# Kernel tuning notes

Measured on AMD Instinct MI355X. Metric: run time of the kernel, lower is better.

The kernel has to match this reference:

```python
import jax, jax.numpy as jnp
import numpy as np

H, Q, D, V = 256, 64, 512, 34
L, N, T = 1024, 64, 256


def _mlp(x, W0, b0, W1, b1):
    # two-layer MLP with ELU on hidden (matches MLP with nn.ELU activation)
    return jax.nn.elu(x @ W0.T + b0) @ W1.T + b1


def _lstm_cell(x, h, c, Wih, Whh, bih, bhh):
    gates = x @ Wih.T + bih + h @ Whh.T + bhh
    i, f, g, o = jnp.split(gates, 4, axis=-1)  # PyTorch LSTMCell gate order
    i, f, o = jax.nn.sigmoid(i), jax.nn.sigmoid(f), jax.nn.sigmoid(o)
    c_new = f * c + i * jnp.tanh(g)
    h_new = o * jnp.tanh(c_new)
    return h_new, c_new


def _attn(q, key, value, mask):
    # q: [N,Q], key: [N,L,Q], value: [N,L,H], mask: [N,L]
    scores = jnp.einsum('nlq,nq->nl', key, q)
    a = jax.nn.softmax(scores, axis=-1) * mask
    a = a / jnp.sum(a, axis=-1, keepdims=True)
    return jnp.einsum('nl,nlh->nh', a, value)


def setup_inputs() -> dict:
    key = jax.random.key(0)
    ks = iter(jax.random.split(key, 64))

    def rn(shape, s=0.05):
        return jax.random.normal(next(ks), shape, jnp.float32) * s

    inp = {
        'seqs': rn((L, N, D), 1.0),
        'seq_lens': jax.random.randint(next(ks), (N,), L // 2, L + 1),
        'labels': jax.random.randint(next(ks), (T, N), 0, V),
        'emb': rn((V, H)),
        'inith': rn((3, H)),
        'initc': rn((3, H)),
    }
    in_sizes = [2 * H, H, H]
    for i in range(3):
        inp[f'Wih{i}'] = rn((4 * H, in_sizes[i]))
        inp[f'Whh{i}'] = rn((4 * H, H))
        inp[f'bih{i}'] = rn((4 * H,))
        inp[f'bhh{i}'] = rn((4 * H,))
    inp['qW0'] = rn((H, H)); inp['qb0'] = rn((H,))
    inp['qW1'] = rn((Q, H)); inp['qb1'] = rn((Q,))
    inp['kW0'] = rn((D, D)); inp['kb0'] = rn((D,))
    inp['kW1'] = rn((Q, D)); inp['kb1'] = rn((Q,))
    inp['vW0'] = rn((H, D)); inp['vb0'] = rn((H,))
    inp['vW1'] = rn((H, H)); inp['vb1'] = rn((H,))
    inp['outW'] = rn((V, 2 * H)); inp['outb'] = rn((V,))
    return inp


def reference(seqs, seq_lens, labels, emb, inith, initc,
              Wih0, Whh0, bih0, bhh0, Wih1, Whh1, bih1, bhh1,
              Wih2, Whh2, bih2, bhh2,
              qW0, qb0, qW1, qb1, kW0, kb0, kW1, kb1,
              vW0, vb0, vW1, vb1, outW, outb):
    T_, N_ = labels.shape
    L_ = seqs.shape[0]
    lstm = [(Wih0, Whh0, bih0, bhh0), (Wih1, Whh1, bih1, bhh1), (Wih2, Whh2, bih2, bhh2)]

    char_input = emb[labels]                                   # [T,N,H]
    key = _mlp(seqs, kW0, kb0, kW1, kb1).transpose(1, 0, 2)    # [N,L,Q]
    value = _mlp(seqs, vW0, vb0, vW1, vb1).transpose(1, 0, 2)  # [N,L,H]
    mask = (jnp.arange(L_)[None, :] < seq_lens[:, None]).astype(seqs.dtype)

    h = jnp.tile(inith[:, None, :], (1, N_, 1))  # [3,N,H]
    c = jnp.tile(initc[:, None, :], (1, N_, 1))
    q = _mlp(h[2], qW0, qb0, qW1, qb1)
    prev_ctx = _attn(q, key, value, mask)

    def step(carry, x_t):
        h, c, ctx = carry
        xin = jnp.concatenate([ctx, x_t], axis=1)  # [N,2H]
        hs, cs = [], []
        for i in range(3):
            nh, nc = _lstm_cell(xin, h[i], c[i], *lstm[i])
            hs.append(nh); cs.append(nc)
            xin = nh
        h = jnp.stack(hs); c = jnp.stack(cs)
        q = _mlp(h[2], qW0, qb0, qW1, qb1)
        ctx = _attn(q, key, value, mask)
        out = jnp.concatenate([ctx, h[2]], axis=1) @ outW.T + outb  # [N,V]
        return (h, c, ctx), out

    _, outs = jax.lax.scan(step, (h, c, prev_ctx), char_input)
    return outs  # [T,N,V]
```

## Files before the change

### kernel.cpp

```cpp
#include <hip/hip_runtime.h>
#include <cstddef>

#define DEV static __device__ __forceinline__
typedef unsigned long long ull;

DEV float b2f(unsigned short u){ unsigned int i=((unsigned int)u)<<16; float f; __builtin_memcpy(&f,&i,4); return f; }
DEV float lo16(unsigned int u){ unsigned int i=u<<16; float f; __builtin_memcpy(&f,&i,4); return f; }
DEV float hi16(unsigned int u){ unsigned int i=u&0xffff0000u; float f; __builtin_memcpy(&f,&i,4); return f; }
DEV unsigned short f2b(float f){ unsigned int i; __builtin_memcpy(&i,&f,4); unsigned int r=(i+0x7fffu+((i>>16)&1u))>>16; return (unsigned short)r; }
DEV float sigf(float x){ return 1.f/(1.f+__expf(-x)); }
DEV float eluf(float x){ return x>0.f ? x : (__expf(x)-1.f); }
DEV float gload(const void* p, long i, int f32){
  return f32 ? ((const float*)p)[i] : b2f(((const unsigned short*)p)[i]);
}
DEV ull pk(float f, unsigned tag){ unsigned b; __builtin_memcpy(&b,&f,4); return ((ull)tag<<32)|b; }
DEV float upk(ull u){ unsigned b=(unsigned)u; float f; __builtin_memcpy(&f,&b,4); return f; }
DEV void ast64(ull* p, ull v){ __hip_atomic_store(p, v, __ATOMIC_RELAXED, __HIP_MEMORY_SCOPE_AGENT); }
DEV ull ald64(const ull* p){ return __hip_atomic_load(p, __ATOMIC_RELAXED, __HIP_MEMORY_SCOPE_AGENT); }

__global__ __launch_bounds__(64) void sniff(const void* __restrict__ seqs,
                                            const void* __restrict__ seq_lens,
                                            int* __restrict__ flags)
{
  __shared__ int cnt;
  if (threadIdx.x==0) cnt=0;
  __syncthreads();
  const unsigned short* u = (const unsigned short*)seqs;
  int sane=0;
  for (int i=threadIdx.x;i<1024;i+=64){
    int e = (u[i]>>7)&0xFF;
    if (e>=0x70 && e<=0x8F) sane++;
  }
  atomicAdd(&cnt, sane);
  __syncthreads();
  if (threadIdx.x==0){
    flags[0] = (cnt < 820) ? 1 : 0;
    const int* s = (const int*)seq_lens;
    flags[1] = ((s[1]|s[3]|s[5]|s[7])==0) ? 1 : 0;
  }
}

__global__ __launch_bounds__(256) void prep_transpose(
    const void* __restrict__ Wih0, const void* __restrict__ Whh0,
    const void* __restrict__ Wih1, const void* __restrict__ Whh1,
    const void* __restrict__ Wih2, const void* __restrict__ Whh2,
    const void* __restrict__ kW0,  const void* __restrict__ kW1,
    const void* __restrict__ vW0,  const void* __restrict__ vW1,
    const void* __restrict__ qW0,  const void* __restrict__ qW1,
    const void* __restrict__ bih0, const void* __restrict__ bhh0,
    const void* __restrict__ bih1, const void* __restrict__ bhh1,
    const void* __restrict__ bih2, const void* __restrict__ bhh2,
    const void* __restrict__ outW, const void* __restrict__ inith,
    const void* __restrict__ initc, const void* __restrict__ qb0,
    const void* __restrict__ qb1,  const void* __restrict__ outb,
    const int* __restrict__ flags,
    unsigned short* __restrict__ Wl0, unsigned short* __restrict__ Wl1,
    unsigned short* __restrict__ Wl2,
    unsigned short* __restrict__ kW0T, unsigned short* __restrict__ kW1T,
    unsigned short* __restrict__ vW0T, unsigned short* __restrict__ vW1T,
    unsigned short* __restrict__ qW0v, unsigned short* __restrict__ qW1v,
    float* __restrict__ bsum,
    unsigned short* __restrict__ outWc, unsigned short* __restrict__ inithc,
    unsigned short* __restrict__ initcc, unsigned short* __restrict__ qb0c,
    unsigned short* __restrict__ qb1c,  unsigned short* __restrict__ outbc)
{
  const int f32 = flags[0];
  int idx = blockIdx.x*256 + threadIdx.x;
  if (idx < 524288){ int r=idx&131071, k=r>>8, gi=r&255;
    int g = ((gi>>6)<<8) + ((idx>>17)<<6) + (gi&63);
    Wl0[idx] = f2b((k<256)? gload(Wih0,(long)g*512+k,f32) : gload(Whh0,(long)g*256+(k-256),f32)); return; }
  idx -= 524288;
  if (idx < 524288){ int r=idx&131071, k=r>>8, gi=r&255;
    int g = ((gi>>6)<<8) + ((idx>>17)<<6) + (gi&63);
    Wl1[idx] = f2b((k<256)? gload(Wih1,(long)g*256+k,f32) : gload(Whh1,(long)g*256+(k-256),f32)); return; }
  idx -= 524288;
  if (idx < 524288){ int r=idx&131071, k=r>>8, gi=r&255;
    int g = ((gi>>6)<<8) + ((idx>>17)<<6) + (gi&63);
    Wl2[idx] = f2b((k<256)? gload(Wih2,(long)g*256+k,f32) : gload(Whh2,(long)g*256+(k-256),f32)); return; }
  idx -= 524288;
  if (idx < 262144){ int k=idx>>9, j=idx&511; kW0T[idx]=f2b(gload(kW0,(long)j*512+k,f32)); return; }
  idx -= 262144;
  if (idx < 32768){ int k=idx>>6, j=idx&63; kW1T[idx]=f2b(gload(kW1,(long)j*512+k,f32)); return; }
  idx -= 32768;
  if (idx < 131072){ int k=idx>>8, j=idx&255; vW0T[idx]=f2b(gload(vW0,(long)j*512+k,f32)); return; }
  idx -= 131072;
  if (idx < 65536){ int k=idx>>8, j=idx&255; vW1T[idx]=f2b(gload(vW1,(long)j*256+k,f32)); return; }
  idx -= 65536;
  if (idx < 65536){
    int k8=idx>>11, j=(idx>>3)&255, kk=idx&7; int k=k8*8+kk;
    qW0v[idx]=f2b(gload(qW0,(long)j*256+k,f32)); return; }
  idx -= 65536;
  if (idx < 16384){
    int k8=idx>>11, qc=(idx>>5)&63, kk=idx&31; int k=k8*32+kk;
    qW1v[idx]=f2b(gload(qW1,(long)qc*256+k,f32)); return; }
  idx -= 16384;
  if (idx < 3072){ int l=idx>>10, r=idx&1023, pp=r>>8, gi=r&255;
    int g = ((gi>>6)<<8) + (pp<<6) + (gi&63);
    const void* bi = (l==0)?bih0:((l==1)?bih1:bih2);
    const void* bh = (l==0)?bhh0:((l==1)?bhh1:bhh2);
    bsum[idx] = gload(bi,g,f32)+gload(bh,g,f32); return; }
  idx -= 3072;
  if (idx < 17408){ outWc[idx]=f2b(gload(outW,idx,f32)); return; }
  idx -= 17408;
  if (idx < 768){ inithc[idx]=f2b(gload(inith,idx,f32)); return; }
  idx -= 768;
  if (idx < 768){ initcc[idx]=f2b(gload(initc,idx,f32)); return; }
  idx -= 768;
  if (idx < 256){ qb0c[idx]=f2b(gload(qb0,idx,f32)); return; }
  idx -= 256;
  if (idx < 64){ qb1c[idx]=f2b(gload(qb1,idx,f32)); return; }
  idx -= 64;
  if (idx < 34){ outbc[idx]=f2b(gload(outb,idx,f32)); return; }
}

__global__ __launch_bounds__(256) void prep_ge(
    const void* __restrict__ emb,
    const void* __restrict__ Wih0,
    const int* __restrict__ flags,
    float* __restrict__ gep)
{
  __shared__ float ev[256];
  const int f32 = flags[0];
  const int v = blockIdx.x, tid = threadIdx.x;
  ev[tid] = gload(emb,(long)v*256+tid,f32);
  __syncthreads();
  #pragma unroll
  for (int j=0;j<4;j++){
    const int g = tid*4+j;
    float a = 0.f;
    #pragma unroll 4
    for (int k=0;k<256;k++) a += ev[k]*gload(Wih0,(long)g*512+256+k,f32);
    int pp = (g>>6)&3, gi = ((g>>8)<<6)|(g&63);
    gep[((size_t)pp*34+v)*256+gi] = a;
  }
}

__global__ __launch_bounds__(256) void key_mlp(
    const void* __restrict__ seqs,
    const unsigned short* __restrict__ kW0T, const void* __restrict__ kb0,
    const unsigned short* __restrict__ kW1T, const void* __restrict__ kb1,
    const int* __restrict__ flags,
    unsigned short* __restrict__ keyT)
{
  __shared__ float Xt[16*512];
  __shared__ unsigned short Hd[16*512];
  const int f32 = flags[0];
  const int tid = threadIdx.x;
  const int R0 = blockIdx.x*16;
  for (int i=tid;i<8192;i+=256) Xt[i] = gload(seqs,(long)R0*512+i,f32);
  __syncthreads();
  {
    const int j0 = 2*tid;
    float acc0[16], acc1[16];
    #pragma unroll
    for (int r=0;r<16;r++){ acc0[r]=0.f; acc1[r]=0.f; }
    for (int k=0;k<512;k++){
      ushort2 w = *reinterpret_cast<const ushort2*>(kW0T + (size_t)k*512 + j0);
      float w0=b2f(w.x), w1=b2f(w.y);
      #pragma unroll
      for (int r=0;r<16;r++){ float x = Xt[r*512+k]; acc0[r]+=x*w0; acc1[r]+=x*w1; }
    }
    float b0v=gload(kb0,j0,f32), b1v=gload(kb0,j0+1,f32);
    #pragma unroll
    for (int r=0;r<16;r++){
      Hd[r*512+j0]   = f2b(eluf(acc0[r]+b0v));
      Hd[r*512+j0+1] = f2b(eluf(acc1[r]+b1v));
    }
  }
  __syncthreads();
  {
    const int j = tid & 63;
    const int rbase = tid >> 6;
    float acc[4] = {0.f,0.f,0.f,0.f};
    for (int k=0;k<512;k++){
      float w = b2f(kW1T[(size_t)k*64 + j]);
      #pragma unroll
      for (int m=0;m<4;m++) acc[m] += b2f(Hd[(rbase+4*m)*512 + k]) * w;
    }
    float bv = gload(kb1,j,f32);
    #pragma unroll
    for (int m=0;m<4;m++){
      int R = R0 + rbase + 4*m;
      int l = R >> 6, n = R & 63;
      keyT[((size_t)(n*64 + j))*1024 + l] = f2b(acc[m]+bv);
    }
  }
}

__global__ __launch_bounds__(256) void value_mlp(
    const void* __restrict__ seqs,
    const unsigned short* __restrict__ vW0T, const void* __restrict__ vb0,
    const unsigned short* __restrict__ vW1T, const void* __restrict__ vb1,
    const int* __restrict__ flags,
    unsigned short* __restrict__ value)
{
  __shared__ float Xt[16*512];
  __shared__ float Hd[16*256];
  const int f32 = flags[0];
  const int tid = threadIdx.x;
  const int R0 = blockIdx.x*16;
  for (int i=tid;i<8192;i+=256) Xt[i] = gload(seqs,(long)R0*512+i,f32);
  __syncthreads();
  {
    const int j0 = 2*(tid & 127);
    const int rh = tid >> 7;
    float acc0[8], acc1[8];
    #pragma unroll
    for (int r=0;r<8;r++){ acc0[r]=0.f; acc1[r]=0.f; }
    for (int k=0;k<512;k++){
      ushort2 w = *reinterpret_cast<const ushort2*>(vW0T + (size_t)k*256 + j0);
      float w0=b2f(w.x), w1=b2f(w.y);
      #pragma unroll
      for (int r=0;r<8;r++){ float x = Xt[(rh*8+r)*512+k]; acc0[r]+=x*w0; acc1[r]+=x*w1; }
    }
    float b0v=gload(vb0,j0,f32), b1v=gload(vb0,j0+1,f32);
    #pragma unroll
    for (int r=0;r<8;r++){
      Hd[(rh*8+r)*256+j0]   = eluf(acc0[r]+b0v);
      Hd[(rh*8+r)*256+j0+1] = eluf(acc1[r]+b1v);
    }
  }
  __syncthreads();
  {
    const int j = tid;
    float acc[16];
    #pragma unroll
    for (int r=0;r<16;r++) acc[r]=0.f;
    for (int k=0;k<256;k++){
      float w = b2f(vW1T[(size_t)k*256 + j]);
      #pragma unroll
      for (int r=0;r<16;r++) acc[r] += Hd[r*256+k]*w;
    }
    float bv = gload(vb1,j,f32);
    #pragma unroll
    for (int r=0;r<16;r++){
      int R = R0 + r; int l = R>>6, n = R&63;
      value[((size_t)n*1024 + l)*256 + j] = f2b(acc[r]+bv);
    }
  }
}

__global__ __launch_bounds__(256) void zero_hbuf(ull* __restrict__ f){
  int i = blockIdx.x*256 + threadIdx.x;
  if (i < 115200) f[i] = 0;
}

__global__ __launch_bounds__(512, 1) void speller(
    const unsigned short* __restrict__ keyT,
    const unsigned short* __restrict__ value,
    const unsigned short* __restrict__ Wl0,
    const unsigned short* __restrict__ Wl1,
    const unsigned short* __restrict__ Wl2,
    const unsigned short* __restrict__ qW0v,
    const unsigned short* __restrict__ qW1v,
    const float* __restrict__ bsum_p,
    const float* __restrict__ gep,
    const unsigned short* __restrict__ inithc,
    const unsigned short* __restrict__ initcc,
    const unsigned short* __restrict__ qb0c,
    const unsigned short* __restrict__ qb1c,
    const unsigned short* __restrict__ outWc,
    const unsigned short* __restrict__ outbc,
    const int* __restrict__ labels,
    const int* __restrict__ seq_lens,
    const int* __restrict__ dflags,
    ull* __restrict__ hbw,
    void* __restrict__ out)
{
  extern __shared__ char smem_dyn[];
  unsigned short* vlds = (unsigned short*)smem_dyn;

  __shared__ float sacc[4096];
  __shared__ float inc[512];
  __shared__ float garr[256];
  __shared__ float h0[256], h1[256], h2[256], ctx[256];
  __shared__ float cloc[3][64];
  __shared__ float hsl[3][64];
  __shared__ float xq[256];
  __shared__ float qv[64];
  __shared__ float earr[256];
  __shared__ float red[16];
  __shared__ float wf[4];
  __shared__ float pcl[256];
  __shared__ float statl[8];

  const int tid = threadIdx.x;
  const int n = blockIdx.x >> 2;
  const int p = blockIdx.x & 3;
  const int f32o = dflags[0];
  const int i64 = dflags[1];
  const int slen = i64 ? seq_lens[2*n] : seq_lens[n];

  ull* mb   = hbw + (size_t)n*1800;
  ull* H0w  = mb;
  ull* H1w  = mb + 256;
  ull* H2w  = mb + 512;
  ull* PCw  = mb + 768;
  ull* STw  = mb + 1792;

  {
    const uint4* src = (const uint4*)(value + ((size_t)n*1024 + p*256)*256);
    uint4* dst = (uint4*)vlds;
    for (int i=tid;i<16384;i+=512) dst[i] = src[i];
  }
  if (tid < 256){ h0[tid]=b2f(inithc[tid]); h1[tid]=b2f(inithc[256+tid]); h2[tid]=b2f(inithc[512+tid]); }
  if (tid < 64){
    cloc[0][tid]=b2f(initcc[p*64+tid]);
    cloc[1][tid]=b2f(initcc[256+p*64+tid]);
    cloc[2][tid]=b2f(initcc[512+p*64+tid]);
  }
  __syncthreads();

  auto lstm = [&](const unsigned short* W, const float* bs, const float* ger,
                  int layer, ull* Hw, unsigned tag){
    const int go8 = tid & 31, ks = tid >> 5;
    const unsigned short* wp = W + (size_t)p*131072 + (size_t)ks*32*256 + go8*8;
    const float* xin = inc + ks*32;
    float a0=0.f,a1=0.f,a2=0.f,a3=0.f,a4=0.f,a5=0.f,a6=0.f,a7=0.f;
    #pragma unroll 16
    for (int k=0;k<32;k++){
      float x = xin[k];
      uint4 w = *reinterpret_cast<const uint4*>(wp + (size_t)k*256);
      a0 += x*lo16(w.x); a1 += x*hi16(w.x);
      a2 += x*lo16(w.y); a3 += x*hi16(w.y);
      a4 += x*lo16(w.z); a5 += x*hi16(w.z);
      a6 += x*lo16(w.w); a7 += x*hi16(w.w);
    }
    float* sb = sacc + ks*256 + go8*8;
    sb[0]=a0; sb[1]=a1; sb[2]=a2; sb[3]=a3; sb[4]=a4; sb[5]=a5; sb[6]=a6; sb[7]=a7;
    __syncthreads();
    if (tid < 256){
      float s = bs[tid] + (ger ? ger[tid] : 0.f);
      #pragma unroll
      for (int u=0;u<16;u++) s += sacc[u*256+tid];
      garr[tid] = s;
    }
    __syncthreads();
    if (tid < 64){
      float gi=garr[tid], gf=garr[64+tid], gg=garr[128+tid], go=garr[192+tid];
      float cc = sigf(gf)*cloc[layer][tid] + sigf(gi)*tanhf(gg);
      float hh = sigf(go)*tanhf(cc);
      cloc[layer][tid]=cc;
      hsl[layer][tid]=hh;
      ast64(Hw + p*64 + tid, pk(hh, tag));
    }
  };

  auto gather_h = [&](const ull* Hw, int layer, unsigned tag, float* hdst,
                      const float* nexth){
    __syncthreads();
    if (tid < 256){
      int sp = tid >> 6; float v;
      if (sp == p) v = hsl[layer][tid & 63];
      else { const ull* w = Hw + tid; ull u = ald64(w);
             while ((unsigned)(u>>32) != tag) u = ald64(w);
             v = upk(u); }
      hdst[tid] = v;
      if (nexth){ inc[tid] = v; inc[256+tid] = nexth[tid]; }
    }
    __syncthreads();
  };

  auto attn = [&](unsigned tag){
    {
      const int j = tid & 255, kh = tid >> 8;
      const uint4* qp = (const uint4*)qW0v + (size_t)(kh*16)*256 + j;
      float a = 0.f;
      #pragma unroll
      for (int k8=0;k8<16;k8++){
        uint4 w = qp[(size_t)k8*256];
        const float* hb = h2 + kh*128 + k8*8;
        a += hb[0]*lo16(w.x)+hb[1]*hi16(w.x)
           + hb[2]*lo16(w.y)+hb[3]*hi16(w.y)
           + hb[4]*lo16(w.z)+hb[5]*hi16(w.z)
           + hb[6]*lo16(w.w)+hb[7]*hi16(w.w);
      }
      sacc[kh*256 + j] = a;
    }
    __syncthreads();
    if (tid < 256) xq[tid] = eluf(sacc[tid]+sacc[256+tid] + b2f(qb0c[tid]));
    __syncthreads();
    {
      const int qc = tid & 63, k8 = tid >> 6;
      const uint4* qp = (const uint4*)qW1v + (size_t)(k8*64+qc)*4;
      float a = 0.f;
      #pragma unroll
      for (int u=0;u<4;u++){
        uint4 w = qp[u];
        const float* xb = xq + k8*32 + u*8;
        a += xb[0]*lo16(w.x)+xb[1]*hi16(w.x)
           + xb[2]*lo16(w.y)+xb[3]*hi16(w.y)
           + xb[4]*lo16(w.z)+xb[5]*hi16(w.z)
           + xb[6]*lo16(w.w)+xb[7]*hi16(w.w);
      }
      sacc[k8*64+qc] = a;
    }
    __syncthreads();
    if (tid < 64){
      float s=0.f;
      #pragma unroll
      for (int u=0;u<8;u++) s += sacc[u*64+tid];
      qv[tid] = s + b2f(qb1c[tid]);
    }
    __syncthreads();
    {
      const int lp = tid & 127, qh = tid >> 7;
      float a0=0.f,a1=0.f;
      const unsigned short* kp = keyT + (size_t)n*65536 + (size_t)qh*16*1024 + p*256 + 2*lp;
      #pragma unroll 8
      for (int q=0;q<16;q++){
        ushort2 w = *reinterpret_cast<const ushort2*>(kp + (size_t)q*1024);
        float qq = qv[qh*16+q];
        a0 += qq*b2f(w.x); a1 += qq*b2f(w.y);
      }
      sacc[qh*256+2*lp]=a0; sacc[qh*256+2*lp+1]=a1;
    }
    __syncthreads();
    float pmax, psum;
    {
      float s = -1e30f;
      if (tid < 256){
        s = sacc[tid]+sacc[256+tid]+sacc[512+tid]+sacc[768+tid];
        if (p*256+tid >= slen) s = -1e30f;
      }
      float m = s;
      #pragma unroll
      for (int off=32; off; off>>=1) m = fmaxf(m, __shfl_xor(m, off));
      if ((tid&63)==0) red[tid>>6] = m;
      __syncthreads();
      pmax = fmaxf(fmaxf(red[0],red[1]),fmaxf(red[2],red[3]));
      float e = 0.f;
      if (tid < 256){
        e = (p*256+tid < slen) ? __expf(s - pmax) : 0.f;
        earr[tid] = e;
      }
      float ss = e;
      #pragma unroll
      for (int off=32; off; off>>=1) ss += __shfl_xor(ss, off);
      if ((tid&63)==0) red[8+(tid>>6)] = ss;
      __syncthreads();
      psum = red[8]+red[9]+red[10]+red[11];
    }
    {
      const int hp = tid & 127, lq = tid >> 7;
      float a0=0.f,a1=0.f;
      const unsigned short* vp = vlds + (size_t)(lq*64)*256 + 2*hp;
      #pragma unroll 8
      for (int l=0;l<64;l++){
        ushort2 w = *reinterpret_cast<const ushort2*>(vp + (size_t)l*256);
        float e = earr[lq*64+l];
        a0 += e*b2f(w.x); a1 += e*b2f(w.y);
      }
      sacc[lq*256+2*hp]=a0; sacc[lq*256+2*hp+1]=a1;
    }
    __syncthreads();
    if (tid < 256){
      float v = sacc[tid]+sacc[256+tid]+sacc[512+tid]+sacc[768+tid];
      pcl[tid] = v;
      ast64(PCw + p*256 + tid, pk(v, tag));
    }
    if (tid == 0){ ast64(STw + p*2, pk(pmax, tag)); ast64(STw + p*2 + 1, pk(psum, tag)); }
    if (tid < 8){
      int q = tid >> 1, ix = tid & 1; float v;
      if (q == p) v = ix ? psum : pmax;
      else { const ull* w = STw + q*2 + ix; ull u = ald64(w);
             while ((unsigned)(u>>32) != tag) u = ald64(w);
             v = upk(u); }
      statl[tid] = v;
    }
    __syncthreads();
    if (tid == 0){
      float m0=statl[0], s0=statl[1], m1=statl[2], s1=statl[3];
      float m2=statl[4], s2=statl[5], m3=statl[6], s3=statl[7];
      float M = fmaxf(fmaxf(m0,m1),fmaxf(m2,m3));
      float w0=__expf(m0-M), w1=__expf(m1-M), w2=__expf(m2-M), w3=__expf(m3-M);
      float inv = 1.f/(s0*w0+s1*w1+s2*w2+s3*w3);
      wf[0]=w0*inv; wf[1]=w1*inv; wf[2]=w2*inv; wf[3]=w3*inv;
    }
    __syncthreads();
    if (tid < 256){
      const int q0=(p+1)&3, q1=(p+2)&3, q2=(p+3)&3;
      const ull* w0 = PCw + q0*256 + tid;
      const ull* w1 = PCw + q1*256 + tid;
      const ull* w2 = PCw + q2*256 + tid;
      ull u0=ald64(w0), u1=ald64(w1), u2=ald64(w2);
      while ((unsigned)(u0>>32) != tag) u0 = ald64(w0);
      while ((unsigned)(u1>>32) != tag) u1 = ald64(w1);
      while ((unsigned)(u2>>32) != tag) u2 = ald64(w2);
      float acc = pcl[tid]*wf[p] + upk(u0)*wf[q0] + upk(u1)*wf[q1] + upk(u2)*wf[q2];
      ctx[tid] = acc;
      inc[tid] = acc;
      inc[256+tid] = h0[tid];
    }
    __syncthreads();
  };

  attn(1);

  for (int t=0;t<256;t++){
    const unsigned tb = 4*(unsigned)t;
    const int lab = i64 ? labels[2*(t*64+n)] : labels[t*64+n];
    lstm(Wl0, bsum_p + p*256, gep + ((size_t)p*34+lab)*256, 0, H0w, tb+2);
    gather_h(H0w, 0, tb+2, h0, h1);
    lstm(Wl1, bsum_p + 1024 + p*256, nullptr, 1, H1w, tb+3);
    gather_h(H1w, 1, tb+3, h1, h2);
    lstm(Wl2, bsum_p + 2048 + p*256, nullptr, 2, H2w, tb+4);
    gather_h(H2w, 2, tb+4, h2, nullptr);
    attn(tb+5);
    {
      const int ri = tid >> 6, kk = tid & 63;
      const int r = 4*ri + p;
      float acc = 0.f;
      const unsigned short* wr = outWc + (size_t)r*512 + kk;
      #pragma unroll
      for (int s=0;s<4;s++) acc += ctx[s*64+kk]*b2f(wr[s*64]);
      #pragma unroll
      for (int s=0;s<4;s++) acc += h2[s*64+kk]*b2f(wr[256+s*64]);
      #pragma unroll
      for (int off=32; off>0; off>>=1) acc += __shfl_down(acc, off);
      if (kk==0){
        float v = acc + b2f(outbc[r]);
        size_t oi = ((size_t)(t*64+n))*34 + r;
        if (f32o) ((float*)out)[oi]=v; else ((unsigned short*)out)[oi]=f2b(v);
      }
      if (p < 2 && tid < 64){
        const int r2 = 32+p;
        float a2=0.f;
        const unsigned short* wr2 = outWc + (size_t)r2*512 + tid;
        #pragma unroll
        for (int s=0;s<4;s++) a2 += ctx[s*64+tid]*b2f(wr2[s*64]);
        #pragma unroll
        for (int s=0;s<4;s++) a2 += h2[s*64+tid]*b2f(wr2[256+s*64]);
        #pragma unroll
        for (int off=32; off>0; off>>=1) a2 += __shfl_down(a2, off);
        if (tid==0){
          float v = a2 + b2f(outbc[r2]);
          size_t oi = ((size_t)(t*64+n))*34 + r2;
          if (f32o) ((float*)out)[oi]=v; else ((unsigned short*)out)[oi]=f2b(v);
        }
      }
    }
  }
}

extern "C" void kernel_launch(void* const* d_in, const int* in_sizes, int n_in,
                              void* d_out, int out_size, void* d_ws, size_t ws_size,
                              hipStream_t stream) {
  const void* seqs  = d_in[0];
  const int* seq_lens = (const int*)d_in[1];
  const int* labels   = (const int*)d_in[2];
  const void* emb   = d_in[3];
  const void* inith = d_in[4];
  const void* initc = d_in[5];
  const void* Wih0 = d_in[6];  const void* Whh0 = d_in[7];
  const void* bih0 = d_in[8];  const void* bhh0 = d_in[9];
  const void* Wih1 = d_in[10]; const void* Whh1 = d_in[11];
  const void* bih1 = d_in[12]; const void* bhh1 = d_in[13];
  const void* Wih2 = d_in[14]; const void* Whh2 = d_in[15];
  const void* bih2 = d_in[16]; const void* bhh2 = d_in[17];
  const void* qW0 = d_in[18];  const void* qb0 = d_in[19];
  const void* qW1 = d_in[20];  const void* qb1 = d_in[21];
  const void* kW0 = d_in[22];  const void* kb0 = d_in[23];
  const void* kW1 = d_in[24];  const void* kb1 = d_in[25];
  const void* vW0 = d_in[26];  const void* vb0 = d_in[27];
  const void* vW1 = d_in[28];  const void* vb1 = d_in[29];
  const void* outW = d_in[30]; const void* outb = d_in[31];

  char* ws = (char*)d_ws;
  unsigned short* keyT  = (unsigned short*)(ws);
  unsigned short* value = (unsigned short*)(ws + 8388608);
  unsigned short* Wl0   = (unsigned short*)(ws + 41943040);
  unsigned short* Wl1   = (unsigned short*)(ws + 42991616);
  unsigned short* Wl2   = (unsigned short*)(ws + 44040192);
  unsigned short* kW0T  = (unsigned short*)(ws + 45088768);
  unsigned short* kW1T  = (unsigned short*)(ws + 45613056);
  unsigned short* vW0T  = (unsigned short*)(ws + 45678592);
  unsigned short* vW1T  = (unsigned short*)(ws + 45940736);
  unsigned short* qW0v  = (unsigned short*)(ws + 46071808);
  unsigned short* qW1v  = (unsigned short*)(ws + 46202880);
  float*          bsum  = (float*)(ws + 46235648);
  float*          gep   = (float*)(ws + 46247936);
  unsigned short* outWc = (unsigned short*)(ws + 46387200);
  unsigned short* inithc= (unsigned short*)(ws + 46422016);
  unsigned short* initcc= (unsigned short*)(ws + 46423552);
  unsigned short* qb0c  = (unsigned short*)(ws + 46425088);
  unsigned short* qb1c  = (unsigned short*)(ws + 46425600);
  unsigned short* outbc = (unsigned short*)(ws + 46425728);
  int*            dflags= (int*)(ws + 46425856);
  ull* hbw = (ull*)(ws + 45088768);

  sniff<<<dim3(1), dim3(64), 0, stream>>>(seqs, seq_lens, dflags);
  prep_transpose<<<dim3(8472), dim3(256), 0, stream>>>(
      Wih0,Whh0,Wih1,Whh1,Wih2,Whh2, kW0,kW1,vW0,vW1,qW0,qW1,
      bih0,bhh0,bih1,bhh1,bih2,bhh2,
      outW,inith,initc,qb0,qb1,outb, dflags,
      Wl0,Wl1,Wl2,kW0T,kW1T,vW0T,vW1T,qW0v,qW1v,bsum,
      outWc,inithc,initcc,qb0c,qb1c,outbc);
  prep_ge<<<dim3(34), dim3(256), 0, stream>>>(emb, Wih0, dflags, gep);
  key_mlp<<<dim3(4096), dim3(256), 0, stream>>>(seqs, kW0T, kb0, kW1T, kb1, dflags, keyT);
  value_mlp<<<dim3(4096), dim3(256), 0, stream>>>(seqs, vW0T, vb0, vW1T, vb1, dflags, value);
  zero_hbuf<<<dim3(450), dim3(256), 0, stream>>>(hbw);
  hipFuncSetAttribute((const void*)speller, hipFuncAttributeMaxDynamicSharedMemorySize, 131072);
  speller<<<dim3(256), dim3(512), 131072, stream>>>(
      keyT, value, Wl0, Wl1, Wl2, qW0v, qW1v, bsum, gep,
      inithc, initcc, qb0c, qb1c, outWc, outbc, labels, seq_lens, dflags,
      hbw, d_out);
}
```

Baseline: 8.160 ms.

## Double speller block to 1024 threads and re-split per-step matvecs

Raises the recurrent speller kernel from 512 to 1024 threads per block. The LSTM gate matvec, the query MLP, the key-score and the value-context reductions are re-partitioned so each thread handles half as many elements, and the partial-sum reductions grow accordingly. The qW1 weight layout in prep is changed to match the new split. The aim is to cut per-step latency on the serial time loop by using more lanes, at the cost of extra shared-memory reduction work and heavier barriers across 16 waves. It also risks register pressure under the tighter launch bound.

```diff
diff --git a/kernel.cpp b/kernel.cpp
--- a/kernel.cpp
+++ b/kernel.cpp
@@ -91,7 +91,7 @@
     qW0v[idx]=f2b(gload(qW0,(long)j*256+k,f32)); return; }
   idx -= 65536;
   if (idx < 16384){
-    int k8=idx>>11, qc=(idx>>5)&63, kk=idx&31; int k=k8*32+kk;
+    int s=idx>>10, qc=(idx>>4)&63, kk=idx&15; int k=s*16+kk;
     qW1v[idx]=f2b(gload(qW1,(long)qc*256+k,f32)); return; }
   idx -= 16384;
   if (idx < 3072){ int l=idx>>10, r=idx&1023, pp=r>>8, gi=r&255;
@@ -245,7 +245,7 @@
   if (i < 115200) f[i] = 0;
 }
 
-__global__ __launch_bounds__(512, 1) void speller(
+__global__ __launch_bounds__(1024, 4) void speller(
     const unsigned short* __restrict__ keyT,
     const unsigned short* __restrict__ value,
     const unsigned short* __restrict__ Wl0,
@@ -301,7 +301,7 @@
   {
     const uint4* src = (const uint4*)(value + ((size_t)n*1024 + p*256)*256);
     uint4* dst = (uint4*)vlds;
-    for (int i=tid;i<16384;i+=512) dst[i] = src[i];
+    for (int i=tid;i<16384;i+=1024) dst[i] = src[i];
   }
   if (tid < 256){ h0[tid]=b2f(inithc[tid]); h1[tid]=b2f(inithc[256+tid]); h2[tid]=b2f(inithc[512+tid]); }
   if (tid < 64){
@@ -313,21 +313,19 @@
 
   auto lstm = [&](const unsigned short* W, const float* bs, const float* ger,
                   int layer, ull* Hw, unsigned tag){
-    const int go8 = tid & 31, ks = tid >> 5;
-    const unsigned short* wp = W + (size_t)p*131072 + (size_t)ks*32*256 + go8*8;
+    const int g4 = tid & 63, ks = tid >> 6;
+    const unsigned short* wp = W + (size_t)p*131072 + (size_t)ks*32*256 + g4*4;
     const float* xin = inc + ks*32;
-    float a0=0.f,a1=0.f,a2=0.f,a3=0.f,a4=0.f,a5=0.f,a6=0.f,a7=0.f;
+    float a0=0.f,a1=0.f,a2=0.f,a3=0.f;
     #pragma unroll 16
     for (int k=0;k<32;k++){
       float x = xin[k];
-      uint4 w = *reinterpret_cast<const uint4*>(wp + (size_t)k*256);
+      uint2 w = *reinterpret_cast<const uint2*>(wp + (size_t)k*256);
       a0 += x*lo16(w.x); a1 += x*hi16(w.x);
       a2 += x*lo16(w.y); a3 += x*hi16(w.y);
-      a4 += x*lo16(w.z); a5 += x*hi16(w.z);
-      a6 += x*lo16(w.w); a7 += x*hi16(w.w);
-    }
-    float* sb = sacc + ks*256 + go8*8;
-    sb[0]=a0; sb[1]=a1; sb[2]=a2; sb[3]=a3; sb[4]=a4; sb[5]=a5; sb[6]=a6; sb[7]=a7;
+    }
+    float* sb = sacc + ks*256 + g4*4;
+    sb[0]=a0; sb[1]=a1; sb[2]=a2; sb[3]=a3;
     __syncthreads();
     if (tid < 256){
       float s = bs[tid] + (ger ? ger[tid] : 0.f);
@@ -364,12 +362,12 @@
   auto attn = [&](unsigned tag){
     {
       const int j = tid & 255, kh = tid >> 8;
-      const uint4* qp = (const uint4*)qW0v + (size_t)(kh*16)*256 + j;
+      const uint4* qp = (const uint4*)qW0v + (size_t)(kh*8)*256 + j;
       float a = 0.f;
       #pragma unroll
-      for (int k8=0;k8<16;k8++){
+      for (int k8=0;k8<8;k8++){
         uint4 w = qp[(size_t)k8*256];
-        const float* hb = h2 + kh*128 + k8*8;
+        const float* hb = h2 + kh*64 + k8*8;
         a += hb[0]*lo16(w.x)+hb[1]*hi16(w.x)
            + hb[2]*lo16(w.y)+hb[3]*hi16(w.y)
            + hb[4]*lo16(w.z)+hb[5]*hi16(w.z)
@@ -378,39 +376,39 @@
       sacc[kh*256 + j] = a;
     }
     __syncthreads();
-    if (tid < 256) xq[tid] = eluf(sacc[tid]+sacc[256+tid] + b2f(qb0c[tid]));
+    if (tid < 256) xq[tid] = eluf(sacc[tid]+sacc[256+tid]+sacc[512+tid]+sacc[768+tid] + b2f(qb0c[tid]));
     __syncthreads();
     {
-      const int qc = tid & 63, k8 = tid >> 6;
-      const uint4* qp = (const uint4*)qW1v + (size_t)(k8*64+qc)*4;
+      const int qc = tid & 63, s = tid >> 6;
+      const uint4* qp = (const uint4*)qW1v + (size_t)(s*64+qc)*2;
       float a = 0.f;
       #pragma unroll
-      for (int u=0;u<4;u++){
+      for (int u=0;u<2;u++){
         uint4 w = qp[u];
-        const float* xb = xq + k8*32 + u*8;
+        const float* xb = xq + s*16 + u*8;
         a += xb[0]*lo16(w.x)+xb[1]*hi16(w.x)
            + xb[2]*lo16(w.y)+xb[3]*hi16(w.y)
            + xb[4]*lo16(w.z)+xb[5]*hi16(w.z)
            + xb[6]*lo16(w.w)+xb[7]*hi16(w.w);
       }
-      sacc[k8*64+qc] = a;
+      sacc[s*64+qc] = a;
     }
     __syncthreads();
     if (tid < 64){
       float s=0.f;
       #pragma unroll
-      for (int u=0;u<8;u++) s += sacc[u*64+tid];
+      for (int u=0;u<16;u++) s += sacc[u*64+tid];
       qv[tid] = s + b2f(qb1c[tid]);
     }
     __syncthreads();
     {
       const int lp = tid & 127, qh = tid >> 7;
       float a0=0.f,a1=0.f;
-      const unsigned short* kp = keyT + (size_t)n*65536 + (size_t)qh*16*1024 + p*256 + 2*lp;
-      #pragma unroll 8
-      for (int q=0;q<16;q++){
+      const unsigned short* kp = keyT + (size_t)n*65536 + (size_t)qh*8*1024 + p*256 + 2*lp;
+      #pragma unroll
+      for (int q=0;q<8;q++){
         ushort2 w = *reinterpret_cast<const ushort2*>(kp + (size_t)q*1024);
-        float qq = qv[qh*16+q];
+        float qq = qv[qh*8+q];
         a0 += qq*b2f(w.x); a1 += qq*b2f(w.y);
       }
       sacc[qh*256+2*lp]=a0; sacc[qh*256+2*lp+1]=a1;
@@ -420,13 +418,14 @@
     {
       float s = -1e30f;
       if (tid < 256){
-        s = sacc[tid]+sacc[256+tid]+sacc[512+tid]+sacc[768+tid];
+        s = sacc[tid]+sacc[256+tid]+sacc[512+tid]+sacc[768+tid]
+          + sacc[1024+tid]+sacc[1280+tid]+sacc[1536+tid]+sacc[1792+tid];
         if (p*256+tid >= slen) s = -1e30f;
       }
       float m = s;
       #pragma unroll
       for (int off=32; off; off>>=1) m = fmaxf(m, __shfl_xor(m, off));
-      if ((tid&63)==0) red[tid>>6] = m;
+      if (tid < 256 && (tid&63)==0) red[tid>>6] = m;
       __syncthreads();
       pmax = fmaxf(fmaxf(red[0],red[1]),fmaxf(red[2],red[3]));
       float e = 0.f;
@@ -437,25 +436,26 @@
       float ss = e;
       #pragma unroll
       for (int off=32; off; off>>=1) ss += __shfl_xor(ss, off);
-      if ((tid&63)==0) red[8+(tid>>6)] = ss;
+      if (tid < 256 && (tid&63)==0) red[8+(tid>>6)] = ss;
       __syncthreads();
       psum = red[8]+red[9]+red[10]+red[11];
     }
     {
       const int hp = tid & 127, lq = tid >> 7;
       float a0=0.f,a1=0.f;
-      const unsigned short* vp = vlds + (size_t)(lq*64)*256 + 2*hp;
+      const unsigned short* vp = vlds + (size_t)(lq*32)*256 + 2*hp;
       #pragma unroll 8
-      for (int l=0;l<64;l++){
+      for (int l=0;l<32;l++){
         ushort2 w = *reinterpret_cast<const ushort2*>(vp + (size_t)l*256);
-        float e = earr[lq*64+l];
+        float e = earr[lq*32+l];
         a0 += e*b2f(w.x); a1 += e*b2f(w.y);
       }
       sacc[lq*256+2*hp]=a0; sacc[lq*256+2*hp+1]=a1;
     }
     __syncthreads();
     if (tid < 256){
-      float v = sacc[tid]+sacc[256+tid]+sacc[512+tid]+sacc[768+tid];
+      float v = sacc[tid]+sacc[256+tid]+sacc[512+tid]+sacc[768+tid]
+              + sacc[1024+tid]+sacc[1280+tid]+sacc[1536+tid]+sacc[1792+tid];
       pcl[tid] = v;
       ast64(PCw + p*256 + tid, pk(v, tag));
     }
@@ -507,7 +507,7 @@
     lstm(Wl2, bsum_p + 2048 + p*256, nullptr, 2, H2w, tb+4);
     gather_h(H2w, 2, tb+4, h2, nullptr);
     attn(tb+5);
-    {
+    if (tid < 512){
       const int ri = tid >> 6, kk = tid & 63;
       const int r = 4*ri + p;
       float acc = 0.f;
@@ -601,7 +601,7 @@
   value_mlp<<<dim3(4096), dim3(256), 0, stream>>>(seqs, vW0T, vb0, vW1T, vb1, dflags, value);
   zero_hbuf<<<dim3(450), dim3(256), 0, stream>>>(hbw);
   hipFuncSetAttribute((const void*)speller, hipFuncAttributeMaxDynamicSharedMemorySize, 131072);
-  speller<<<dim3(256), dim3(512), 131072, stream>>>(
+  speller<<<dim3(256), dim3(1024), 131072, stream>>>(
       keyT, value, Wl0, Wl1, Wl2, qW0v, qW1v, bsum, gep,
       inithc, initcc, qb0c, qb1c, outWc, outbc, labels, seq_lens, dflags,
       hbw, d_out);
```

Result: slower. 13.99 ms (+71.5%).

## Fuse cross-block h polling into LSTM matvec with shuffle broadcast

Applied to the files above, without the earlier changes.

Layers 1 and 2 of the LSTM now poll the previous layer's published h directly inside the matvec. Each wave broadcasts the polled values to its lanes with shuffles instead of first gathering them into shared memory behind an extra barrier. This removes one __syncthreads and one LDS round trip per layer per step. The gate activations are raised in wave priority so their results are published to other blocks sooner, and the qW1 layout is reshuffled for the query MLP second layer. The risk is that waves for different k-slices each spin-wait separately, and the lane mapping and layout changes must still match.

```diff
diff --git a/kernel.cpp b/kernel.cpp
--- a/kernel.cpp
+++ b/kernel.cpp
@@ -91,7 +91,7 @@
     qW0v[idx]=f2b(gload(qW0,(long)j*256+k,f32)); return; }
   idx -= 65536;
   if (idx < 16384){
-    int k8=idx>>11, qc=(idx>>5)&63, kk=idx&31; int k=k8*32+kk;
+    int s=idx>>10, qc=(idx>>4)&63, kk=idx&15; int k=s*16+kk;
     qW1v[idx]=f2b(gload(qW1,(long)qc*256+k,f32)); return; }
   idx -= 16384;
   if (idx < 3072){ int l=idx>>10, r=idx&1023, pp=r>>8, gi=r&255;
@@ -275,7 +275,6 @@
   __shared__ float garr[256];
   __shared__ float h0[256], h1[256], h2[256], ctx[256];
   __shared__ float cloc[3][64];
-  __shared__ float hsl[3][64];
   __shared__ float xq[256];
   __shared__ float qv[64];
   __shared__ float earr[256];
@@ -311,8 +310,8 @@
   }
   __syncthreads();
 
-  auto lstm = [&](const unsigned short* W, const float* bs, const float* ger,
-                  int layer, ull* Hw, unsigned tag){
+  auto lstm_lds = [&](const unsigned short* W, const float* bs, const float* ger,
+                      int layer, ull* Hw, unsigned tag){
     const int go8 = tid & 31, ks = tid >> 5;
     const unsigned short* wp = W + (size_t)p*131072 + (size_t)ks*32*256 + go8*8;
     const float* xin = inc + ks*32;
@@ -337,26 +336,68 @@
     }
     __syncthreads();
     if (tid < 64){
+      __builtin_amdgcn_s_setprio(1);
       float gi=garr[tid], gf=garr[64+tid], gg=garr[128+tid], go=garr[192+tid];
       float cc = sigf(gf)*cloc[layer][tid] + sigf(gi)*tanhf(gg);
       float hh = sigf(go)*tanhf(cc);
       cloc[layer][tid]=cc;
-      hsl[layer][tid]=hh;
       ast64(Hw + p*64 + tid, pk(hh, tag));
+      __builtin_amdgcn_s_setprio(0);
     }
   };
 
-  auto gather_h = [&](const ull* Hw, int layer, unsigned tag, float* hdst,
-                      const float* nexth){
+  auto lstm_poll = [&](const unsigned short* W, const float* bs,
+                       const ull* Xw, unsigned xtag, const float* hprev,
+                       float* xdst, int layer, ull* Hw, unsigned tag){
+    const int go8 = tid & 31, ks = tid >> 5;
+    const int lane = tid & 63, wv = tid >> 6;
+    float xv;
+    if (wv < 4){
+      const ull* wd = Xw + tid;
+      ull u = ald64(wd);
+      while ((unsigned)(u>>32) != xtag) u = ald64(wd);
+      xv = upk(u);
+    } else {
+      xv = hprev[tid - 256];
+    }
+    const unsigned short* wp = W + (size_t)p*131072 + (size_t)ks*32*256 + go8*8;
+    float a0=0.f,a1=0.f,a2=0.f,a3=0.f,a4=0.f,a5=0.f,a6=0.f,a7=0.f;
+    #pragma unroll 16
+    for (int k=0;k<32;k++){
+      float x = __shfl(xv, (lane & 32) | k);
+      uint4 w = *reinterpret_cast<const uint4*>(wp + (size_t)k*256);
+      a0 += x*lo16(w.x); a1 += x*hi16(w.x);
+      a2 += x*lo16(w.y); a3 += x*hi16(w.y);
+      a4 += x*lo16(w.z); a5 += x*hi16(w.z);
+      a6 += x*lo16(w.w); a7 += x*hi16(w.w);
+    }
+    float* sb = sacc + ks*256 + go8*8;
+    sb[0]=a0; sb[1]=a1; sb[2]=a2; sb[3]=a3; sb[4]=a4; sb[5]=a5; sb[6]=a6; sb[7]=a7;
+    if (wv < 4) xdst[tid] = xv;
     __syncthreads();
     if (tid < 256){
-      int sp = tid >> 6; float v;
-      if (sp == p) v = hsl[layer][tid & 63];
-      else { const ull* w = Hw + tid; ull u = ald64(w);
-             while ((unsigned)(u>>32) != tag) u = ald64(w);
-             v = upk(u); }
-      hdst[tid] = v;
-      if (nexth){ inc[tid] = v; inc[256+tid] = nexth[tid]; }
+      float s = bs[tid];
+      #pragma unroll
+      for (int u=0;u<16;u++) s += sacc[u*256+tid];
+      garr[tid] = s;
+    }
+    __syncthreads();
+    if (tid < 64){
+      __builtin_amdgcn_s_setprio(1);
+      float gi=garr[tid], gf=garr[64+tid], gg=garr[128+tid], go=garr[192+tid];
+      float cc = sigf(gf)*cloc[layer][tid] + sigf(gi)*tanhf(gg);
+      float hh = sigf(go)*tanhf(cc);
+      cloc[layer][tid]=cc;
+      ast64(Hw + p*64 + tid, pk(hh, tag));
+      __builtin_amdgcn_s_setprio(0);
+    }
+  };
+
+  auto gather_h2 = [&](unsigned tag){
+    if (tid < 256){
+      const ull* w = H2w + tid; ull u = ald64(w);
+      while ((unsigned)(u>>32) != tag) u = ald64(w);
+      h2[tid] = upk(u);
     }
     __syncthreads();
   };
@@ -381,19 +422,23 @@
     if (tid < 256) xq[tid] = eluf(sacc[tid]+sacc[256+tid] + b2f(qb0c[tid]));
     __syncthreads();
     {
-      const int qc = tid & 63, k8 = tid >> 6;
-      const uint4* qp = (const uint4*)qW1v + (size_t)(k8*64+qc)*4;
+      const int qc = tid & 63, s = tid >> 6;
+      const uint4* qp = (const uint4*)qW1v + (size_t)(2*s*64+qc)*2;
       float a = 0.f;
       #pragma unroll
-      for (int u=0;u<4;u++){
-        uint4 w = qp[u];
-        const float* xb = xq + k8*32 + u*8;
-        a += xb[0]*lo16(w.x)+xb[1]*hi16(w.x)
-           + xb[2]*lo16(w.y)+xb[3]*hi16(w.y)
-           + xb[4]*lo16(w.z)+xb[5]*hi16(w.z)
-           + xb[6]*lo16(w.w)+xb[7]*hi16(w.w);
-      }
-      sacc[k8*64+qc] = a;
+      for (int half=0;half<2;half++){
+        const uint4* qph = qp + (size_t)half*64*2;
+        #pragma unroll
+        for (int u=0;u<2;u++){
+          uint4 w = qph[u];
+          const float* xb = xq + s*32 + half*16 + u*8;
+          a += xb[0]*lo16(w.x)+xb[1]*hi16(w.x)
+             + xb[2]*lo16(w.y)+xb[3]*hi16(w.y)
+             + xb[4]*lo16(w.z)+xb[5]*hi16(w.z)
+             + xb[6]*lo16(w.w)+xb[7]*hi16(w.w);
+        }
+      }
+      sacc[s*64+qc] = a;
     }
     __syncthreads();
     if (tid < 64){
@@ -500,12 +545,10 @@
   for (int t=0;t<256;t++){
     const unsigned tb = 4*(unsigned)t;
     const int lab = i64 ? labels[2*(t*64+n)] : labels[t*64+n];
-    lstm(Wl0, bsum_p + p*256, gep + ((size_t)p*34+lab)*256, 0, H0w, tb+2);
-    gather_h(H0w, 0, tb+2, h0, h1);
-    lstm(Wl1, bsum_p + 1024 + p*256, nullptr, 1, H1w, tb+3);
-    gather_h(H1w, 1, tb+3, h1, h2);
-    lstm(Wl2, bsum_p + 2048 + p*256, nullptr, 2, H2w, tb+4);
-    gather_h(H2w, 2, tb+4, h2, nullptr);
+    lstm_lds(Wl0, bsum_p + p*256, gep + ((size_t)p*34+lab)*256, 0, H0w, tb+2);
+    lstm_poll(Wl1, bsum_p + 1024 + p*256, H0w, tb+2, h1, h0, 1, H1w, tb+3);
+    lstm_poll(Wl2, bsum_p + 2048 + p*256, H1w, tb+3, h2, h1, 2, H2w, tb+4);
+    gather_h2(tb+4);
     attn(tb+5);
     {
       const int ri = tid >> 6, kk = tid & 63;
```

Result: no change. 8.173 ms (+0.2%).

## Relayout LSTM and query weights for per-thread dot products, cache layer-1 weights in registers

Applied to the files above, without the earlier changes.

Rewrites the weight pre-pack so each thread owns one gate row half and streams contiguous 16-byte chunks. Partial sums are then combined with wave shuffles instead of LDS staging and extra barriers, and the gate nonlinearity is done in-wave. Layer-1 LSTM weights are kept resident in 32 uint4 registers per thread across all timesteps, avoiding re-reading them each step. The query MLP gets the same shuffle-reduction treatment. This trades higher register pressure, which may lower occupancy or cause spills, for fewer barriers and less shared-memory traffic.

```diff
diff --git a/kernel.cpp b/kernel.cpp
--- a/kernel.cpp
+++ b/kernel.cpp
@@ -66,16 +66,25 @@
 {
   const int f32 = flags[0];
   int idx = blockIdx.x*256 + threadIdx.x;
-  if (idx < 524288){ int r=idx&131071, k=r>>8, gi=r&255;
-    int g = ((gi>>6)<<8) + ((idx>>17)<<6) + (gi&63);
+  if (idx < 524288){ int pp=idx>>17, r=idx&131071;
+    int it8=r>>12, ln=(r>>3)&511, e=r&7;
+    int j=ln>>3, gi=(ln>>1)&3, half=ln&1;
+    int g = gi*256 + pp*64 + j;
+    int k = half*256 + it8*8 + e;
     Wl0[idx] = f2b((k<256)? gload(Wih0,(long)g*512+k,f32) : gload(Whh0,(long)g*256+(k-256),f32)); return; }
   idx -= 524288;
-  if (idx < 524288){ int r=idx&131071, k=r>>8, gi=r&255;
-    int g = ((gi>>6)<<8) + ((idx>>17)<<6) + (gi&63);
+  if (idx < 524288){ int pp=idx>>17, r=idx&131071;
+    int it8=r>>12, ln=(r>>3)&511, e=r&7;
+    int j=ln>>3, gi=(ln>>1)&3, half=ln&1;
+    int g = gi*256 + pp*64 + j;
+    int k = half*256 + it8*8 + e;
     Wl1[idx] = f2b((k<256)? gload(Wih1,(long)g*256+k,f32) : gload(Whh1,(long)g*256+(k-256),f32)); return; }
   idx -= 524288;
-  if (idx < 524288){ int r=idx&131071, k=r>>8, gi=r&255;
-    int g = ((gi>>6)<<8) + ((idx>>17)<<6) + (gi&63);
+  if (idx < 524288){ int pp=idx>>17, r=idx&131071;
+    int it8=r>>12, ln=(r>>3)&511, e=r&7;
+    int j=ln>>3, gi=(ln>>1)&3, half=ln&1;
+    int g = gi*256 + pp*64 + j;
+    int k = half*256 + it8*8 + e;
     Wl2[idx] = f2b((k<256)? gload(Wih2,(long)g*256+k,f32) : gload(Whh2,(long)g*256+(k-256),f32)); return; }
   idx -= 524288;
   if (idx < 262144){ int k=idx>>9, j=idx&511; kW0T[idx]=f2b(gload(kW0,(long)j*512+k,f32)); return; }
@@ -87,11 +96,13 @@
   if (idx < 65536){ int k=idx>>8, j=idx&255; vW1T[idx]=f2b(gload(vW1,(long)j*256+k,f32)); return; }
   idx -= 65536;
   if (idx < 65536){
-    int k8=idx>>11, j=(idx>>3)&255, kk=idx&7; int k=k8*8+kk;
+    int k8=idx>>12, ln=(idx>>3)&511, e=idx&7;
+    int j=ln>>1, half=ln&1; int k=half*128 + k8*8 + e;
     qW0v[idx]=f2b(gload(qW0,(long)j*256+k,f32)); return; }
   idx -= 65536;
   if (idx < 16384){
-    int k8=idx>>11, qc=(idx>>5)&63, kk=idx&31; int k=k8*32+kk;
+    int g=idx>>12, ln=(idx>>3)&511, e=idx&7;
+    int qc=ln>>3, s8=ln&7; int k=s8*32 + g*8 + e;
     qW1v[idx]=f2b(gload(qW1,(long)qc*256+k,f32)); return; }
   idx -= 16384;
   if (idx < 3072){ int l=idx>>10, r=idx&1023, pp=r>>8, gi=r&255;
@@ -270,12 +281,12 @@
   extern __shared__ char smem_dyn[];
   unsigned short* vlds = (unsigned short*)smem_dyn;
 
-  __shared__ float sacc[4096];
-  __shared__ float inc[512];
-  __shared__ float garr[256];
+  __shared__ float sacc[1024];
+  __shared__ __align__(16) float xb[512];
   __shared__ float h0[256], h1[256], h2[256], ctx[256];
   __shared__ float cloc[3][64];
-  __shared__ float hsl[3][64];
+  __shared__ float hown[3][64];
+  __shared__ float bsl[3][256];
   __shared__ float xq[256];
   __shared__ float qv[64];
   __shared__ float earr[256];
@@ -309,98 +320,125 @@
     cloc[1][tid]=b2f(initcc[256+p*64+tid]);
     cloc[2][tid]=b2f(initcc[512+p*64+tid]);
   }
-  __syncthreads();
-
-  auto lstm = [&](const unsigned short* W, const float* bs, const float* ger,
-                  int layer, ull* Hw, unsigned tag){
-    const int go8 = tid & 31, ks = tid >> 5;
-    const unsigned short* wp = W + (size_t)p*131072 + (size_t)ks*32*256 + go8*8;
-    const float* xin = inc + ks*32;
-    float a0=0.f,a1=0.f,a2=0.f,a3=0.f,a4=0.f,a5=0.f,a6=0.f,a7=0.f;
-    #pragma unroll 16
-    for (int k=0;k<32;k++){
-      float x = xin[k];
-      uint4 w = *reinterpret_cast<const uint4*>(wp + (size_t)k*256);
-      a0 += x*lo16(w.x); a1 += x*hi16(w.x);
-      a2 += x*lo16(w.y); a3 += x*hi16(w.y);
-      a4 += x*lo16(w.z); a5 += x*hi16(w.z);
-      a6 += x*lo16(w.w); a7 += x*hi16(w.w);
-    }
-    float* sb = sacc + ks*256 + go8*8;
-    sb[0]=a0; sb[1]=a1; sb[2]=a2; sb[3]=a3; sb[4]=a4; sb[5]=a5; sb[6]=a6; sb[7]=a7;
-    __syncthreads();
-    if (tid < 256){
-      float s = bs[tid] + (ger ? ger[tid] : 0.f);
-      #pragma unroll
-      for (int u=0;u<16;u++) s += sacc[u*256+tid];
-      garr[tid] = s;
-    }
-    __syncthreads();
-    if (tid < 64){
-      float gi=garr[tid], gf=garr[64+tid], gg=garr[128+tid], go=garr[192+tid];
-      float cc = sigf(gf)*cloc[layer][tid] + sigf(gi)*tanhf(gg);
-      float hh = sigf(go)*tanhf(cc);
-      cloc[layer][tid]=cc;
-      hsl[layer][tid]=hh;
-      ast64(Hw + p*64 + tid, pk(hh, tag));
+  for (int i=tid;i<768;i+=512){ int l=i>>8, gx=i&255; bsl[l][gx]=bsum_p[l*1024 + p*256 + gx]; }
+  uint4 w1r[32];
+  {
+    const unsigned short* wp1 = Wl1 + (size_t)p*131072 + tid*8;
+    #pragma unroll
+    for (int i=0;i<32;i++) w1r[i] = *reinterpret_cast<const uint4*>(wp1 + (size_t)i*4096);
+  }
+  __syncthreads();
+
+  const int half = tid & 1;
+  const int gidx = ((tid>>1)&3)*64 + (tid>>3);
+  const int lb   = (tid & 63) & ~7;
+
+  auto lstm_stream = [&](const unsigned short* W, int layer, const float* ger,
+                         ull* Hw, unsigned tag){
+    const float* xs = xb + half*256;
+    const unsigned short* wp = W + (size_t)p*131072 + tid*8;
+    float a = 0.f;
+    #pragma unroll 8
+    for (int it8=0; it8<32; it8++){
+      uint4 w = *reinterpret_cast<const uint4*>(wp + (size_t)it8*4096);
+      float4 x0 = *reinterpret_cast<const float4*>(xs + it8*8);
+      float4 x1 = *reinterpret_cast<const float4*>(xs + it8*8 + 4);
+      a += x0.x*lo16(w.x)+x0.y*hi16(w.x)+x0.z*lo16(w.y)+x0.w*hi16(w.y)
+         + x1.x*lo16(w.z)+x1.y*hi16(w.z)+x1.z*lo16(w.w)+x1.w*hi16(w.w);
+    }
+    a += __shfl_xor(a, 1);
+    float gsum = a + bsl[layer][gidx] + (ger ? ger[gidx] : 0.f);
+    float g_i = __shfl(gsum, lb+0);
+    float g_f = __shfl(gsum, lb+2);
+    float g_g = __shfl(gsum, lb+4);
+    float g_o = __shfl(gsum, lb+6);
+    if ((tid&7)==0){
+      __builtin_amdgcn_s_setprio(1);
+      int jj = tid>>3;
+      float cc = sigf(g_f)*cloc[layer][jj] + sigf(g_i)*tanhf(g_g);
+      float hh = sigf(g_o)*tanhf(cc);
+      cloc[layer][jj]=cc; hown[layer][jj]=hh;
+      ast64(Hw + p*64 + jj, pk(hh, tag));
+      __builtin_amdgcn_s_setprio(0);
     }
   };
 
-  auto gather_h = [&](const ull* Hw, int layer, unsigned tag, float* hdst,
-                      const float* nexth){
+  auto lstm_reg = [&](int layer, ull* Hw, unsigned tag){
+    const float* xs = xb + half*256;
+    float a = 0.f;
+    #pragma unroll
+    for (int it8=0; it8<32; it8++){
+      uint4 w = w1r[it8];
+      float4 x0 = *reinterpret_cast<const float4*>(xs + it8*8);
+      float4 x1 = *reinterpret_cast<const float4*>(xs + it8*8 + 4);
+      a += x0.x*lo16(w.x)+x0.y*hi16(w.x)+x0.z*lo16(w.y)+x0.w*hi16(w.y)
+         + x1.x*lo16(w.z)+x1.y*hi16(w.z)+x1.z*lo16(w.w)+x1.w*hi16(w.w);
+    }
+    a += __shfl_xor(a, 1);
+    float gsum = a + bsl[layer][gidx];
+    float g_i = __shfl(gsum, lb+0);
+    float g_f = __shfl(gsum, lb+2);
+    float g_g = __shfl(gsum, lb+4);
+    float g_o = __shfl(gsum, lb+6);
+    if ((tid&7)==0){
+      __builtin_amdgcn_s_setprio(1);
+      int jj = tid>>3;
+      float cc = sigf(g_f)*cloc[layer][jj] + sigf(g_i)*tanhf(g_g);
+      float hh = sigf(g_o)*tanhf(cc);
+      cloc[layer][jj]=cc; hown[layer][jj]=hh;
+      ast64(Hw + p*64 + jj, pk(hh, tag));
+      __builtin_amdgcn_s_setprio(0);
+    }
+  };
+
+  auto fill_from = [&](const ull* Hw, unsigned tag, int layer, float* harr,
+                       const float* hnext){
     __syncthreads();
     if (tid < 256){
       int sp = tid >> 6; float v;
-      if (sp == p) v = hsl[layer][tid & 63];
+      if (sp == p) v = hown[layer][tid & 63];
       else { const ull* w = Hw + tid; ull u = ald64(w);
              while ((unsigned)(u>>32) != tag) u = ald64(w);
              v = upk(u); }
-      hdst[tid] = v;
-      if (nexth){ inc[tid] = v; inc[256+tid] = nexth[tid]; }
+      harr[tid] = v;
+      if (hnext){ xb[tid] = v; xb[256+tid] = hnext[tid]; }
     }
     __syncthreads();
   };
 
   auto attn = [&](unsigned tag){
     {
-      const int j = tid & 255, kh = tid >> 8;
-      const uint4* qp = (const uint4*)qW0v + (size_t)(kh*16)*256 + j;
+      const int j = tid>>1;
       float a = 0.f;
       #pragma unroll
       for (int k8=0;k8<16;k8++){
-        uint4 w = qp[(size_t)k8*256];
-        const float* hb = h2 + kh*128 + k8*8;
+        uint4 w = ((const uint4*)qW0v)[k8*512 + tid];
+        const float* hb = h2 + half*128 + k8*8;
         a += hb[0]*lo16(w.x)+hb[1]*hi16(w.x)
            + hb[2]*lo16(w.y)+hb[3]*hi16(w.y)
            + hb[4]*lo16(w.z)+hb[5]*hi16(w.z)
            + hb[6]*lo16(w.w)+hb[7]*hi16(w.w);
       }
-      sacc[kh*256 + j] = a;
-    }
-    __syncthreads();
-    if (tid < 256) xq[tid] = eluf(sacc[tid]+sacc[256+tid] + b2f(qb0c[tid]));
+      a += __shfl_xor(a, 1);
+      if (half==0) xq[j] = eluf(a + b2f(qb0c[j]));
+    }
     __syncthreads();
     {
-      const int qc = tid & 63, k8 = tid >> 6;
-      const uint4* qp = (const uint4*)qW1v + (size_t)(k8*64+qc)*4;
+      const int qc = tid>>3, s8 = tid&7;
       float a = 0.f;
       #pragma unroll
-      for (int u=0;u<4;u++){
-        uint4 w = qp[u];
-        const float* xb = xq + k8*32 + u*8;
-        a += xb[0]*lo16(w.x)+xb[1]*hi16(w.x)
-           + xb[2]*lo16(w.y)+xb[3]*hi16(w.y)
-           + xb[4]*lo16(w.z)+xb[5]*hi16(w.z)
-           + xb[6]*lo16(w.w)+xb[7]*hi16(w.w);
-      }
-      sacc[k8*64+qc] = a;
-    }
-    __syncthreads();
-    if (tid < 64){
-      float s=0.f;
-      #pragma unroll
-      for (int u=0;u<8;u++) s += sacc[u*64+tid];
-      qv[tid] = s + b2f(qb1c[tid]);
+      for (int g=0;g<4;g++){
+        uint4 w = ((const uint4*)qW1v)[g*512 + tid];
+        const float* xs8 = xq + s8*32 + g*8;
+        a += xs8[0]*lo16(w.x)+xs8[1]*hi16(w.x)
+           + xs8[2]*lo16(w.y)+xs8[3]*hi16(w.y)
+           + xs8[4]*lo16(w.z)+xs8[5]*hi16(w.z)
+           + xs8[6]*lo16(w.w)+xs8[7]*hi16(w.w);
+      }
+      a += __shfl_xor(a, 1);
+      a += __shfl_xor(a, 2);
+      a += __shfl_xor(a, 4);
+      if (s8==0) qv[qc] = a + b2f(qb1c[qc]);
     }
     __syncthreads();
     {
@@ -489,8 +527,8 @@
       while ((unsigned)(u2>>32) != tag) u2 = ald64(w2);
       float acc = pcl[tid]*wf[p] + upk(u0)*wf[q0] + upk(u1)*wf[q1] + upk(u2)*wf[q2];
       ctx[tid] = acc;
-      inc[tid] = acc;
-      inc[256+tid] = h0[tid];
+      xb[tid] = acc;
+      xb[256+tid] = h0[tid];
     }
     __syncthreads();
   };
@@ -500,12 +538,13 @@
   for (int t=0;t<256;t++){
     const unsigned tb = 4*(unsigned)t;
     const int lab = i64 ? labels[2*(t*64+n)] : labels[t*64+n];
-    lstm(Wl0, bsum_p + p*256, gep + ((size_t)p*34+lab)*256, 0, H0w, tb+2);
-    gather_h(H0w, 0, tb+2, h0, h1);
-    lstm(Wl1, bsum_p + 1024 + p*256, nullptr, 1, H1w, tb+3);
-    gather_h(H1w, 1, tb+3, h1, h2);
-    lstm(Wl2, bsum_p + 2048 + p*256, nullptr, 2, H2w, tb+4);
-    gather_h(H2w, 2, tb+4, h2, nullptr);
+    const float* ger = gep + ((size_t)p*34+lab)*256;
+    lstm_stream(Wl0, 0, ger, H0w, tb+2);
+    fill_from(H0w, tb+2, 0, h0, h1);
+    lstm_reg(1, H1w, tb+3);
+    fill_from(H1w, tb+3, 1, h1, h2);
+    lstm_stream(Wl2, 2, nullptr, H2w, tb+4);
+    fill_from(H2w, tb+4, 2, h2, nullptr);
     attn(tb+5);
     {
       const int ri = tid >> 6, kk = tid & 63;
```

Result: slower. 28.12 ms (+244.7%).
